# Kernel tuning notes

Measured on AMD Instinct MI355X. Metric: run time of the kernel, lower is better.

The kernel has to match this reference:

```python
import jax, jax.numpy as jnp
import numpy as np

B, S, D = 64, 2048, 64

def setup_inputs() -> dict:
    key = jax.random.key(0)
    k1, k2, k3, k4 = jax.random.split(key, 4)
    query = jax.random.normal(k1, (B, S, D), dtype=jnp.float32)
    keyt = jax.random.normal(k2, (B, S, D), dtype=jnp.float32)
    value = jax.random.normal(k3, (B, S, D), dtype=jnp.float32)
    mask = jax.random.randint(k4, (1, S, S), 0, 2, dtype=jnp.int32)
    return {"query": query, "key": keyt, "value": value, "mask": mask}

def reference(query, key, value, mask):
    # scores: [B, S, S]
    scale = jnp.sqrt(jnp.asarray(value.shape[-1], dtype=query.dtype))
    scores = jnp.einsum('bqd,bkd->bqk', query, key) / scale
    scores = jnp.where(mask == 0, jnp.asarray(-1e9, dtype=scores.dtype), scores)
    attention_weights = jax.nn.softmax(scores, axis=-1)
    # dropout p=0.0 -> identity
    context = jnp.einsum('bqk,bkd->bqd', attention_weights, value)
    return (context, attention_weights)
```

## Files before the change

### kernel.cpp

```cpp
#include <hip/hip_runtime.h>

#define NB 64
#define NS 2048
#define ND 64
#define KSTEP 64
#define NIT (NS / KSTEP)

typedef __bf16 bf16x8 __attribute__((ext_vector_type(8)));
typedef float f32x4 __attribute__((ext_vector_type(4)));
typedef unsigned int u32;
typedef u32 u32x2 __attribute__((ext_vector_type(2)));
typedef u32 u32x4 __attribute__((ext_vector_type(4)));
typedef unsigned short u16;
typedef u16 u16x8 __attribute__((ext_vector_type(8)));

#define C2F 0.18033688011112042f

__device__ __forceinline__ float fexp2(float x) {
#if __has_builtin(__builtin_amdgcn_exp2f)
  return __builtin_amdgcn_exp2f(x);
#else
  return exp2f(x);
#endif
}
__device__ __forceinline__ float flog2(float x) {
#if __has_builtin(__builtin_amdgcn_logf)
  return __builtin_amdgcn_logf(x);
#else
  return log2f(x);
#endif
}

#define TILE_BARRIER()                                   \
  do {                                                   \
    asm volatile("s_waitcnt lgkmcnt(0)" ::: "memory");   \
    __builtin_amdgcn_s_barrier();                        \
    asm volatile("" ::: "memory");                       \
  } while (0)

__device__ __forceinline__ u16 f2bs(float x) {
  __bf16 h = (__bf16)x;
  return __builtin_bit_cast(u16, h);
}

__device__ __forceinline__ bf16x8 cvt8(f32x4 a, f32x4 b) {
  bf16x8 r;
  r[0] = (__bf16)a[0]; r[1] = (__bf16)a[1]; r[2] = (__bf16)a[2]; r[3] = (__bf16)a[3];
  r[4] = (__bf16)b[0]; r[5] = (__bf16)b[1]; r[6] = (__bf16)b[2]; r[7] = (__bf16)b[3];
  return r;
}

__global__ __launch_bounds__(256) void prep_cast_k(const float* __restrict__ K,
                                                   u16* __restrict__ Kbf) {
  const size_t i = ((size_t)blockIdx.x * 256 + threadIdx.x) * 8;
  f32x4 a = __builtin_nontemporal_load((const f32x4*)(K + i));
  f32x4 b = __builtin_nontemporal_load((const f32x4*)(K + i + 4));
  *(bf16x8*)(Kbf + i) = cvt8(a, b);
}

__global__ __launch_bounds__(256) void prep_transp_v(const float* __restrict__ V,
                                                     u16* __restrict__ VT) {
  __shared__ __attribute__((aligned(16))) u16 T[64][72];
  const int b = blockIdx.x >> 5, kt = blockIdx.x & 31;
  const float* src = V + ((size_t)b * NS + kt * 64) * ND;
  {
    const int k = threadIdx.x >> 2, d0 = (threadIdx.x & 3) * 16;
    const float* p = src + (size_t)k * ND + d0;
    f32x4 a0 = __builtin_nontemporal_load((const f32x4*)p);
    f32x4 a1 = __builtin_nontemporal_load((const f32x4*)(p + 4));
    f32x4 a2 = __builtin_nontemporal_load((const f32x4*)(p + 8));
    f32x4 a3 = __builtin_nontemporal_load((const f32x4*)(p + 12));
    *(bf16x8*)&T[k][d0]     = cvt8(a0, a1);
    *(bf16x8*)&T[k][d0 + 8] = cvt8(a2, a3);
  }
  __syncthreads();
  const int d = threadIdx.x >> 2, k0 = (threadIdx.x & 3) * 16;
  u16x8 r0, r1;
#pragma unroll
  for (int j = 0; j < 8; ++j) {
    const int P0 = k0 + j, P1 = k0 + 8 + j;
    const int s0 = 32 * (P0 >> 5) + 16 * ((P0 >> 2) & 1) + 4 * ((P0 >> 3) & 3) + (P0 & 3);
    const int s1 = 32 * (P1 >> 5) + 16 * ((P1 >> 2) & 1) + 4 * ((P1 >> 3) & 3) + (P1 & 3);
    r0[j] = T[s0][d];
    r1[j] = T[s1][d];
  }
  u16* dst = VT + ((size_t)b * ND + d) * NS + kt * 64 + k0;
  *(u16x8*)dst = r0;
  *(u16x8*)(dst + 8) = r1;
}

__global__ __launch_bounds__(256) void prep_pack_mask(const int* __restrict__ M,
                                                      unsigned long long* __restrict__ Mb) {
  const size_t i = (size_t)blockIdx.x * 256 + threadIdx.x;
  const unsigned long long bal = __ballot(M[i] != 0);
  if ((threadIdx.x & 63) == 0) Mb[i >> 6] = bal;
}

template <bool PRE>
__global__ __launch_bounds__(512, 3) void DotProductAttention_22436909154804_kernel(
    const float* __restrict__ Q, const float* __restrict__ K,
    const float* __restrict__ V, const int* __restrict__ M,
    const u16* __restrict__ Kbf, const u16* __restrict__ VTbf,
    const u32* __restrict__ Mb, float* __restrict__ ctx, float* __restrict__ wts) {
  __shared__ __attribute__((aligned(16))) u16 Kt[2][64][72];
  __shared__ __attribute__((aligned(16))) u16 Vt[2][64][72];
  __shared__ float Rs[2][64];

  const int tid  = threadIdx.x;
  const int lane = tid & 63;
  const int w    = tid >> 6;
  const int wq   = w & 3;
  const int kt   = w >> 2;
  const int g    = lane >> 4;
  const int c    = lane & 15;

  const int bid = blockIdx.x;
  const int vb  = (bid & 7) * 256 + (bid >> 3);
  const int b   = vb >> 5;
  const int qt  = vb & 31;
  const int q0w = qt * 64 + wq * 16;
  const size_t bq = (size_t)b * NS;

  const float* qp = Q + (bq + q0w + c) * ND + 8 * g;
  f32x4 qa = __builtin_nontemporal_load((const f32x4*)qp);
  f32x4 qb = __builtin_nontemporal_load((const f32x4*)(qp + 4));
  const bf16x8 qf0 = cvt8(qa, qb);
  qa = __builtin_nontemporal_load((const f32x4*)(qp + 32));
  qb = __builtin_nontemporal_load((const f32x4*)(qp + 36));
  const bf16x8 qf1 = cvt8(qa, qb);

  const u16* Kbb = PRE ? (Kbf + bq * ND) : (const u16*)nullptr;
  const u16* VTb = PRE ? (VTbf + bq * ND) : (const u16*)nullptr;
  const float* Kb32 = K + bq * ND;
  const float* Vb32 = V + bq * ND;
  const int* Mr  = M + (size_t)(q0w + c) * NS + kt * 32;
  const u32* Mbr = Mb + (size_t)(q0w + c) * (NS / 32) + kt;

  const bool isK = tid < 256;
  const int st   = tid & 255;

  auto msel = [](float e, u32 mm, int idx) -> float {
    u32 keep = (u32)(((int)(mm << (31 - idx))) >> 31);
    return __uint_as_float(__float_as_uint(e) & keep);
  };

  u16x8 sp0, sp1;
  f32x4 kf0, kf1, kf2, kf3;
  auto issueK1 = [&](int kb) {
    if (PRE) {
      const int r = tid >> 3, cc = (tid & 7) * 8;
      sp0 = *(const u16x8*)(Kbb + (size_t)(kb + r) * ND + cc);
    } else if (isK) {
      const int r = st >> 2, cc = (st & 3) * 16;
      const float* p = Kb32 + (size_t)(kb + r) * ND + cc;
      kf0 = *(const f32x4*)p;       kf1 = *(const f32x4*)(p + 4);
      kf2 = *(const f32x4*)(p + 8); kf3 = *(const f32x4*)(p + 12);
    }
  };
  auto writeK1 = [&](int buf) {
    if (PRE) {
      const int r = tid >> 3, cc = (tid & 7) * 8;
      *(u16x8*)&Kt[buf][r][cc] = sp0;
    } else if (isK) {
      const int r = st >> 2, cc = (st & 3) * 16;
      *(bf16x8*)&Kt[buf][r][cc]     = cvt8(kf0, kf1);
      *(bf16x8*)&Kt[buf][r][cc + 8] = cvt8(kf2, kf3);
    }
  };
  auto issueKV = [&](int kb) {
    if (PRE) {
      if (isK) {
        const int r = st >> 2, cc = (st & 3) * 16;
        const u16* p = Kbb + (size_t)(kb + r) * ND + cc;
        sp0 = *(const u16x8*)p; sp1 = *(const u16x8*)(p + 8);
      } else {
        const int d = st >> 2, kc = (st & 3) * 16;
        const u16* p = VTb + (size_t)d * NS + kb + kc;
        sp0 = *(const u16x8*)p; sp1 = *(const u16x8*)(p + 8);
      }
    } else {
      if (isK) {
        const int r = st >> 2, cc = (st & 3) * 16;
        const float* p = Kb32 + (size_t)(kb + r) * ND + cc;
        kf0 = *(const f32x4*)p;       kf1 = *(const f32x4*)(p + 4);
        kf2 = *(const f32x4*)(p + 8); kf3 = *(const f32x4*)(p + 12);
      } else {
        const int k = st >> 2, d0 = (st & 3) * 16;
        const float* p = Vb32 + (size_t)(kb + k) * ND + d0;
        kf0 = *(const f32x4*)p;       kf1 = *(const f32x4*)(p + 4);
        kf2 = *(const f32x4*)(p + 8); kf3 = *(const f32x4*)(p + 12);
      }
    }
  };
  auto writeKV = [&](int buf) {
    if (PRE) {
      if (isK) {
        const int r = st >> 2, cc = (st & 3) * 16;
        *(u16x8*)&Kt[buf][r][cc] = sp0; *(u16x8*)&Kt[buf][r][cc + 8] = sp1;
      } else {
        const int d = st >> 2, kc = (st & 3) * 16;
        *(u16x8*)&Vt[buf][d][kc] = sp0; *(u16x8*)&Vt[buf][d][kc + 8] = sp1;
      }
    } else {
      if (isK) {
        const int r = st >> 2, cc = (st & 3) * 16;
        *(bf16x8*)&Kt[buf][r][cc]     = cvt8(kf0, kf1);
        *(bf16x8*)&Kt[buf][r][cc + 8] = cvt8(kf2, kf3);
      } else {
        const int k = st >> 2, d0 = (st & 3) * 16;
        bf16x8 v0 = cvt8(kf0, kf1), v1 = cvt8(kf2, kf3);
#pragma unroll
        for (int j = 0; j < 8; ++j) {
          Vt[buf][d0 + j][k]     = __builtin_bit_cast(u16, v0[j]);
          Vt[buf][d0 + 8 + j][k] = __builtin_bit_cast(u16, v1[j]);
        }
      }
    }
  };

  const f32x4 zz = {0.f, 0.f, 0.f, 0.f};

  float rs = 0.f;
  issueK1(0);
  writeK1(0);
  __syncthreads();
  for (int it = 0; it < NIT; ++it) {
    const int cur = it & 1, kb = it * KSTEP;
    if (it + 1 < NIT) issueK1(kb + KSTEP);
    u32 mm = 0;
    if (PRE) mm = Mbr[kb >> 5];
#pragma unroll
    for (int j = 0; j < 2; ++j) {
      bf16x8 a0 = *(const bf16x8*)&Kt[cur][kt * 32 + 16 * j + c][8 * g];
      bf16x8 a1 = *(const bf16x8*)&Kt[cur][kt * 32 + 16 * j + c][32 + 8 * g];
      f32x4 s = __builtin_amdgcn_mfma_f32_16x16x32_bf16(a0, qf0, zz, 0, 0, 0);
      s = __builtin_amdgcn_mfma_f32_16x16x32_bf16(a1, qf1, s, 0, 0, 0);
      if (PRE) {
        rs += msel(fexp2(s[0] * C2F), mm, 16 * j + 4 * g + 0)
            + msel(fexp2(s[1] * C2F), mm, 16 * j + 4 * g + 1)
            + msel(fexp2(s[2] * C2F), mm, 16 * j + 4 * g + 2)
            + msel(fexp2(s[3] * C2F), mm, 16 * j + 4 * g + 3);
      } else {
        const int4 m4 = *(const int4*)(Mr + kb + 16 * j + 4 * g);
        rs += (m4.x ? fexp2(s[0] * C2F) : 0.f)
            + (m4.y ? fexp2(s[1] * C2F) : 0.f)
            + (m4.z ? fexp2(s[2] * C2F) : 0.f)
            + (m4.w ? fexp2(s[3] * C2F) : 0.f);
      }
    }
    if (it + 1 < NIT) writeK1((it + 1) & 1);
    TILE_BARRIER();
  }
  rs += __shfl_xor(rs, 16);
  rs += __shfl_xor(rs, 32);
  issueKV(0);
  if (lane < 16) Rs[kt][wq * 16 + c] = rs;
  __syncthreads();
  const float l2inv = -flog2(Rs[0][wq * 16 + c] + Rs[1][wq * 16 + c]);
  writeKV(0);
  __syncthreads();

  f32x4 acc[4] = {zz, zz, zz, zz};
  float* wrow = wts + (bq + q0w + c) * NS + kt * 32;
  for (int it = 0; it < NIT; ++it) {
    const int cur = it & 1, kb = it * KSTEP;
    if (it + 1 < NIT) issueKV(kb + KSTEP);
    u32 mm = 0;
    if (PRE) mm = Mbr[kb >> 5];

    u32 wpk[4];
#pragma unroll
    for (int j = 0; j < 2; ++j) {
      bf16x8 a0 = *(const bf16x8*)&Kt[cur][kt * 32 + 16 * j + c][8 * g];
      bf16x8 a1 = *(const bf16x8*)&Kt[cur][kt * 32 + 16 * j + c][32 + 8 * g];
      f32x4 s = __builtin_amdgcn_mfma_f32_16x16x32_bf16(a0, qf0, zz, 0, 0, 0);
      s = __builtin_amdgcn_mfma_f32_16x16x32_bf16(a1, qf1, s, 0, 0, 0);
      float w0, w1, w2, w3;
      if (PRE) {
        w0 = msel(fexp2(fmaf(s[0], C2F, l2inv)), mm, 16 * j + 4 * g + 0);
        w1 = msel(fexp2(fmaf(s[1], C2F, l2inv)), mm, 16 * j + 4 * g + 1);
        w2 = msel(fexp2(fmaf(s[2], C2F, l2inv)), mm, 16 * j + 4 * g + 2);
        w3 = msel(fexp2(fmaf(s[3], C2F, l2inv)), mm, 16 * j + 4 * g + 3);
      } else {
        const int4 m4 = *(const int4*)(Mr + kb + 16 * j + 4 * g);
        w0 = m4.x ? fexp2(fmaf(s[0], C2F, l2inv)) : 0.f;
        w1 = m4.y ? fexp2(fmaf(s[1], C2F, l2inv)) : 0.f;
        w2 = m4.z ? fexp2(fmaf(s[2], C2F, l2inv)) : 0.f;
        w3 = m4.w ? fexp2(fmaf(s[3], C2F, l2inv)) : 0.f;
      }
      f32x4 wv = {w0, w1, w2, w3};
      __builtin_nontemporal_store(wv, (f32x4*)(wrow + kb + 16 * j + 4 * g));
      wpk[2 * j]     = (u32)f2bs(w0) | ((u32)f2bs(w1) << 16);
      wpk[2 * j + 1] = (u32)f2bs(w2) | ((u32)f2bs(w3) << 16);
    }

    u32x4 wu = {wpk[0], wpk[1], wpk[2], wpk[3]};
    bf16x8 wb = __builtin_bit_cast(bf16x8, wu);
#pragma unroll
    for (int dt = 0; dt < 4; ++dt) {
      bf16x8 va;
      if (PRE) {
        va = *(const bf16x8*)&Vt[cur][dt * 16 + c][kt * 32 + 8 * g];
      } else {
        u32x2 vlo = *(const u32x2*)&Vt[cur][dt * 16 + c][kt * 32 + 4 * g];
        u32x2 vhi = *(const u32x2*)&Vt[cur][dt * 16 + c][kt * 32 + 16 + 4 * g];
        u32x4 vau = {vlo.x, vlo.y, vhi.x, vhi.y};
        va = __builtin_bit_cast(bf16x8, vau);
      }
      acc[dt] = __builtin_amdgcn_mfma_f32_16x16x32_bf16(va, wb, acc[dt], 0, 0, 0);
    }

    if (it + 1 < NIT) writeKV((it + 1) & 1);
    TILE_BARRIER();
  }

  float* red = (float*)&Kt[0][0][0] + wq * 1088;
  if (kt == 1) {
#pragma unroll
    for (int dt = 0; dt < 4; ++dt)
      *(f32x4*)&red[c * 68 + dt * 16 + 4 * g] = acc[dt];
  }
  __syncthreads();
  if (kt == 0) {
    float* crow = ctx + (bq + q0w + c) * ND;
#pragma unroll
    for (int dt = 0; dt < 4; ++dt) {
      f32x4 vv = acc[dt] + *(const f32x4*)&red[c * 68 + dt * 16 + 4 * g];
      __builtin_nontemporal_store(vv, (f32x4*)(crow + dt * 16 + 4 * g));
    }
  }
}

extern "C" void kernel_launch(void* const* d_in, const int* in_sizes, int n_in,
                              void* d_out, int out_size, void* d_ws, size_t ws_size,
                              hipStream_t stream) {
  const float* Q = (const float*)d_in[0];
  const float* K = (const float*)d_in[1];
  const float* V = (const float*)d_in[2];
  const int*   M = (const int*)d_in[3];
  float* ctx = (float*)d_out;
  float* wts = (float*)d_out + (size_t)NB * NS * ND;

  dim3 grid(NB * (NS / 64));
  dim3 block(512);

  constexpr size_t KBF_B = (size_t)NB * NS * ND * 2;
  constexpr size_t MB_B  = (size_t)NS * NS / 8;
  u16* Kbf = (u16*)d_ws;
  u16* VTb = (u16*)((char*)d_ws + KBF_B);
  unsigned long long* Mb64 = (unsigned long long*)((char*)d_ws + 2 * KBF_B);

  if (ws_size >= 2 * KBF_B + MB_B) {
    hipLaunchKernelGGL(prep_cast_k, dim3(NB * NS * ND / 8 / 256), dim3(256), 0, stream, K, Kbf);
    hipLaunchKernelGGL(prep_transp_v, dim3(NB * (NS / 64)), dim3(256), 0, stream, V, VTb);
    hipLaunchKernelGGL(prep_pack_mask, dim3(NS * NS / 256), dim3(256), 0, stream, M, Mb64);
    hipLaunchKernelGGL(DotProductAttention_22436909154804_kernel<true>, grid, block, 0, stream,
                       Q, K, V, M, Kbf, VTb, (const u32*)Mb64, ctx, wts);
  } else {
    hipLaunchKernelGGL(DotProductAttention_22436909154804_kernel<false>, grid, block, 0, stream,
                       Q, K, V, M, (const u16*)nullptr, (const u16*)nullptr,
                       (const u32*)nullptr, ctx, wts);
  }
}
```

Baseline: 346.0 us.

## Widen pass-1 key tiles to 128 rows using both K and V smem buffers

In the precomputed-bf16 path, the row-sum pass now loads 128 key rows per iteration instead of 64. It reuses both the Kt and Vt shared buffers as a double-buffered pair, so each warp handles 64 keys per step with a two-word mask load. This halves the number of barrier-separated iterations in pass 1 and gives each thread wider 32-byte loads. The cost is more MFMA/exp work per step and more shared-memory use, with the pass-2 loaders moved below pass 1.

```diff
diff --git a/kernel.cpp b/kernel.cpp
--- a/kernel.cpp
+++ b/kernel.cpp
@@ -133,8 +133,9 @@
   const u16* VTb = PRE ? (VTbf + bq * ND) : (const u16*)nullptr;
   const float* Kb32 = K + bq * ND;
   const float* Vb32 = V + bq * ND;
-  const int* Mr  = M + (size_t)(q0w + c) * NS + kt * 32;
-  const u32* Mbr = Mb + (size_t)(q0w + c) * (NS / 32) + kt;
+  const int* Mr   = M + (size_t)(q0w + c) * NS + kt * 32;
+  const u32* MbRow = Mb + (size_t)(q0w + c) * (NS / 32);
+  const u32* Mbr   = MbRow + kt;
 
   const bool isK = tid < 256;
   const int st   = tid & 255;
@@ -144,115 +145,142 @@
     return __uint_as_float(__float_as_uint(e) & keep);
   };
 
-  u16x8 sp0, sp1;
-  f32x4 kf0, kf1, kf2, kf3;
-  auto issueK1 = [&](int kb) {
-    if (PRE) {
-      const int r = tid >> 3, cc = (tid & 7) * 8;
-      sp0 = *(const u16x8*)(Kbb + (size_t)(kb + r) * ND + cc);
-    } else if (isK) {
-      const int r = st >> 2, cc = (st & 3) * 16;
-      const float* p = Kb32 + (size_t)(kb + r) * ND + cc;
-      kf0 = *(const f32x4*)p;       kf1 = *(const f32x4*)(p + 4);
-      kf2 = *(const f32x4*)(p + 8); kf3 = *(const f32x4*)(p + 12);
-    }
-  };
-  auto writeK1 = [&](int buf) {
-    if (PRE) {
-      const int r = tid >> 3, cc = (tid & 7) * 8;
-      *(u16x8*)&Kt[buf][r][cc] = sp0;
-    } else if (isK) {
-      const int r = st >> 2, cc = (st & 3) * 16;
-      *(bf16x8*)&Kt[buf][r][cc]     = cvt8(kf0, kf1);
-      *(bf16x8*)&Kt[buf][r][cc + 8] = cvt8(kf2, kf3);
-    }
-  };
-  auto issueKV = [&](int kb) {
-    if (PRE) {
-      if (isK) {
-        const int r = st >> 2, cc = (st & 3) * 16;
-        const u16* p = Kbb + (size_t)(kb + r) * ND + cc;
-        sp0 = *(const u16x8*)p; sp1 = *(const u16x8*)(p + 8);
-      } else {
-        const int d = st >> 2, kc = (st & 3) * 16;
-        const u16* p = VTb + (size_t)d * NS + kb + kc;
-        sp0 = *(const u16x8*)p; sp1 = *(const u16x8*)(p + 8);
-      }
-    } else {
+  const f32x4 zz = {0.f, 0.f, 0.f, 0.f};
+  float rs = 0.f;
+
+  if (PRE) {
+    const int r1  = tid >> 2;
+    const int cc1 = (tid & 3) * 16;
+    u16x8 pa, pb;
+    auto issueP1 = [&](int kb) {
+      const u16* p = Kbb + (size_t)(kb + r1) * ND + cc1;
+      pa = *(const u16x8*)p;
+      pb = *(const u16x8*)(p + 8);
+    };
+    auto writeP1 = [&](int pair) {
+      u16(*dst)[72] = pair ? Vt[r1 >> 6] : Kt[r1 >> 6];
+      *(u16x8*)&dst[r1 & 63][cc1]     = pa;
+      *(u16x8*)&dst[r1 & 63][cc1 + 8] = pb;
+    };
+    issueP1(0);
+    writeP1(0);
+    __syncthreads();
+    for (int it = 0; it < 16; ++it) {
+      const int pair = it & 1;
+      if (it + 1 < 16) issueP1((it + 1) * 128);
+      const u32x2 mv = *(const u32x2*)(MbRow + it * 4 + kt * 2);
+      u16(*B)[72] = pair ? Vt[kt] : Kt[kt];
+#pragma unroll
+      for (int j = 0; j < 4; ++j) {
+        bf16x8 a0 = *(const bf16x8*)&B[16 * j + c][8 * g];
+        bf16x8 a1 = *(const bf16x8*)&B[16 * j + c][32 + 8 * g];
+        f32x4 s = __builtin_amdgcn_mfma_f32_16x16x32_bf16(a0, qf0, zz, 0, 0, 0);
+        s = __builtin_amdgcn_mfma_f32_16x16x32_bf16(a1, qf1, s, 0, 0, 0);
+        const u32 mm = (j < 2) ? mv.x : mv.y;
+        const int base = 16 * (j & 1) + 4 * g;
+        rs += msel(fexp2(s[0] * C2F), mm, base + 0)
+            + msel(fexp2(s[1] * C2F), mm, base + 1)
+            + msel(fexp2(s[2] * C2F), mm, base + 2)
+            + msel(fexp2(s[3] * C2F), mm, base + 3);
+      }
+      if (it + 1 < 16) writeP1((it + 1) & 1);
+      TILE_BARRIER();
+    }
+  } else {
+    f32x4 kf0, kf1, kf2, kf3;
+    auto issueK1 = [&](int kb) {
       if (isK) {
         const int r = st >> 2, cc = (st & 3) * 16;
         const float* p = Kb32 + (size_t)(kb + r) * ND + cc;
         kf0 = *(const f32x4*)p;       kf1 = *(const f32x4*)(p + 4);
         kf2 = *(const f32x4*)(p + 8); kf3 = *(const f32x4*)(p + 12);
-      } else {
-        const int k = st >> 2, d0 = (st & 3) * 16;
-        const float* p = Vb32 + (size_t)(kb + k) * ND + d0;
-        kf0 = *(const f32x4*)p;       kf1 = *(const f32x4*)(p + 4);
-        kf2 = *(const f32x4*)(p + 8); kf3 = *(const f32x4*)(p + 12);
-      }
-    }
-  };
-  auto writeKV = [&](int buf) {
-    if (PRE) {
-      if (isK) {
-        const int r = st >> 2, cc = (st & 3) * 16;
-        *(u16x8*)&Kt[buf][r][cc] = sp0; *(u16x8*)&Kt[buf][r][cc + 8] = sp1;
-      } else {
-        const int d = st >> 2, kc = (st & 3) * 16;
-        *(u16x8*)&Vt[buf][d][kc] = sp0; *(u16x8*)&Vt[buf][d][kc + 8] = sp1;
-      }
-    } else {
+      }
+    };
+    auto writeK1 = [&](int buf) {
       if (isK) {
         const int r = st >> 2, cc = (st & 3) * 16;
         *(bf16x8*)&Kt[buf][r][cc]     = cvt8(kf0, kf1);
         *(bf16x8*)&Kt[buf][r][cc + 8] = cvt8(kf2, kf3);
-      } else {
-        const int k = st >> 2, d0 = (st & 3) * 16;
-        bf16x8 v0 = cvt8(kf0, kf1), v1 = cvt8(kf2, kf3);
-#pragma unroll
-        for (int j = 0; j < 8; ++j) {
-          Vt[buf][d0 + j][k]     = __builtin_bit_cast(u16, v0[j]);
-          Vt[buf][d0 + 8 + j][k] = __builtin_bit_cast(u16, v1[j]);
-        }
-      }
-    }
-  };
-
-  const f32x4 zz = {0.f, 0.f, 0.f, 0.f};
-
-  float rs = 0.f;
-  issueK1(0);
-  writeK1(0);
-  __syncthreads();
-  for (int it = 0; it < NIT; ++it) {
-    const int cur = it & 1, kb = it * KSTEP;
-    if (it + 1 < NIT) issueK1(kb + KSTEP);
-    u32 mm = 0;
-    if (PRE) mm = Mbr[kb >> 5];
-#pragma unroll
-    for (int j = 0; j < 2; ++j) {
-      bf16x8 a0 = *(const bf16x8*)&Kt[cur][kt * 32 + 16 * j + c][8 * g];
-      bf16x8 a1 = *(const bf16x8*)&Kt[cur][kt * 32 + 16 * j + c][32 + 8 * g];
-      f32x4 s = __builtin_amdgcn_mfma_f32_16x16x32_bf16(a0, qf0, zz, 0, 0, 0);
-      s = __builtin_amdgcn_mfma_f32_16x16x32_bf16(a1, qf1, s, 0, 0, 0);
-      if (PRE) {
-        rs += msel(fexp2(s[0] * C2F), mm, 16 * j + 4 * g + 0)
-            + msel(fexp2(s[1] * C2F), mm, 16 * j + 4 * g + 1)
-            + msel(fexp2(s[2] * C2F), mm, 16 * j + 4 * g + 2)
-            + msel(fexp2(s[3] * C2F), mm, 16 * j + 4 * g + 3);
-      } else {
+      }
+    };
+    issueK1(0);
+    writeK1(0);
+    __syncthreads();
+    for (int it = 0; it < NIT; ++it) {
+      const int cur = it & 1, kb = it * KSTEP;
+      if (it + 1 < NIT) issueK1(kb + KSTEP);
+#pragma unroll
+      for (int j = 0; j < 2; ++j) {
+        bf16x8 a0 = *(const bf16x8*)&Kt[cur][kt * 32 + 16 * j + c][8 * g];
+        bf16x8 a1 = *(const bf16x8*)&Kt[cur][kt * 32 + 16 * j + c][32 + 8 * g];
+        f32x4 s = __builtin_amdgcn_mfma_f32_16x16x32_bf16(a0, qf0, zz, 0, 0, 0);
+        s = __builtin_amdgcn_mfma_f32_16x16x32_bf16(a1, qf1, s, 0, 0, 0);
         const int4 m4 = *(const int4*)(Mr + kb + 16 * j + 4 * g);
         rs += (m4.x ? fexp2(s[0] * C2F) : 0.f)
             + (m4.y ? fexp2(s[1] * C2F) : 0.f)
             + (m4.z ? fexp2(s[2] * C2F) : 0.f)
             + (m4.w ? fexp2(s[3] * C2F) : 0.f);
       }
-    }
-    if (it + 1 < NIT) writeK1((it + 1) & 1);
-    TILE_BARRIER();
+      if (it + 1 < NIT) writeK1((it + 1) & 1);
+      TILE_BARRIER();
+    }
   }
   rs += __shfl_xor(rs, 16);
   rs += __shfl_xor(rs, 32);
+
+  u16x8 sp0, sp1;
+  f32x4 kf0, kf1, kf2, kf3;
+  auto issueKV = [&](int kb) {
+    if (PRE) {
+      if (isK) {
+        const int r = st >> 2, cc = (st & 3) * 16;
+        const u16* p = Kbb + (size_t)(kb + r) * ND + cc;
+        sp0 = *(const u16x8*)p; sp1 = *(const u16x8*)(p + 8);
+      } else {
+        const int d = st >> 2, kc = (st & 3) * 16;
+        const u16* p = VTb + (size_t)d * NS + kb + kc;
+        sp0 = *(const u16x8*)p; sp1 = *(const u16x8*)(p + 8);
+      }
+    } else {
+      if (isK) {
+        const int r = st >> 2, cc = (st & 3) * 16;
+        const float* p = Kb32 + (size_t)(kb + r) * ND + cc;
+        kf0 = *(const f32x4*)p;       kf1 = *(const f32x4*)(p + 4);
+        kf2 = *(const f32x4*)(p + 8); kf3 = *(const f32x4*)(p + 12);
+      } else {
+        const int k = st >> 2, d0 = (st & 3) * 16;
+        const float* p = Vb32 + (size_t)(kb + k) * ND + d0;
+        kf0 = *(const f32x4*)p;       kf1 = *(const f32x4*)(p + 4);
+        kf2 = *(const f32x4*)(p + 8); kf3 = *(const f32x4*)(p + 12);
+      }
+    }
+  };
+  auto writeKV = [&](int buf) {
+    if (PRE) {
+      if (isK) {
+        const int r = st >> 2, cc = (st & 3) * 16;
+        *(u16x8*)&Kt[buf][r][cc] = sp0; *(u16x8*)&Kt[buf][r][cc + 8] = sp1;
+      } else {
+        const int d = st >> 2, kc = (st & 3) * 16;
+        *(u16x8*)&Vt[buf][d][kc] = sp0; *(u16x8*)&Vt[buf][d][kc + 8] = sp1;
+      }
+    } else {
+      if (isK) {
+        const int r = st >> 2, cc = (st & 3) * 16;
+        *(bf16x8*)&Kt[buf][r][cc]     = cvt8(kf0, kf1);
+        *(bf16x8*)&Kt[buf][r][cc + 8] = cvt8(kf2, kf3);
+      } else {
+        const int k = st >> 2, d0 = (st & 3) * 16;
+        bf16x8 v0 = cvt8(kf0, kf1), v1 = cvt8(kf2, kf3);
+#pragma unroll
+        for (int j = 0; j < 8; ++j) {
+          Vt[buf][d0 + j][k]     = __builtin_bit_cast(u16, v0[j]);
+          Vt[buf][d0 + 8 + j][k] = __builtin_bit_cast(u16, v1[j]);
+        }
+      }
+    }
+  };
+
   issueKV(0);
   if (lane < 16) Rs[kt][wq * 16 + c] = rs;
   __syncthreads();
```

After: 336.1 us (median of 2 runs). -2.8%, faster.

## Read bf16 K directly from global in row-sum pass, splitting keys per kt

Applied to the files above, without the earlier changes.

In the precomputed-bf16 path, the first (row-sum) pass no longer stages K tiles through double-buffered LDS with barriers. Each kt half now loads its own contiguous 1024-key range straight from global memory into MFMA operands and reads the packed mask words sequentially. The aim is to drop the LDS writes, reads and per-iteration barriers from this pass. The cost is uncoalesced, L2-dependent global loads with nothing overlapping their latency. The exp2/log2 helpers are also switched from amdgcn builtins to the standard exp2f/log2f, which may add range-handling instructions.

```diff
diff --git a/kernel.cpp b/kernel.cpp
--- a/kernel.cpp
+++ b/kernel.cpp
@@ -16,20 +16,8 @@
 
 #define C2F 0.18033688011112042f
 
-__device__ __forceinline__ float fexp2(float x) {
-#if __has_builtin(__builtin_amdgcn_exp2f)
-  return __builtin_amdgcn_exp2f(x);
-#else
-  return exp2f(x);
-#endif
-}
-__device__ __forceinline__ float flog2(float x) {
-#if __has_builtin(__builtin_amdgcn_logf)
-  return __builtin_amdgcn_logf(x);
-#else
-  return log2f(x);
-#endif
-}
+__device__ __forceinline__ float fexp2(float x) { return exp2f(x); }
+__device__ __forceinline__ float flog2(float x) { return log2f(x); }
 
 #define TILE_BARRIER()                                   \
   do {                                                   \
@@ -133,8 +121,9 @@
   const u16* VTb = PRE ? (VTbf + bq * ND) : (const u16*)nullptr;
   const float* Kb32 = K + bq * ND;
   const float* Vb32 = V + bq * ND;
-  const int* Mr  = M + (size_t)(q0w + c) * NS + kt * 32;
-  const u32* Mbr = Mb + (size_t)(q0w + c) * (NS / 32) + kt;
+  const int* Mr    = M + (size_t)(q0w + c) * NS + kt * 32;
+  const u32* MbRow = Mb + (size_t)(q0w + c) * (NS / 32);
+  const u32* Mbr   = MbRow + kt;
 
   const bool isK = tid < 256;
   const int st   = tid & 255;
@@ -144,115 +133,123 @@
     return __uint_as_float(__float_as_uint(e) & keep);
   };
 
-  u16x8 sp0, sp1;
-  f32x4 kf0, kf1, kf2, kf3;
-  auto issueK1 = [&](int kb) {
-    if (PRE) {
-      const int r = tid >> 3, cc = (tid & 7) * 8;
-      sp0 = *(const u16x8*)(Kbb + (size_t)(kb + r) * ND + cc);
-    } else if (isK) {
-      const int r = st >> 2, cc = (st & 3) * 16;
-      const float* p = Kb32 + (size_t)(kb + r) * ND + cc;
-      kf0 = *(const f32x4*)p;       kf1 = *(const f32x4*)(p + 4);
-      kf2 = *(const f32x4*)(p + 8); kf3 = *(const f32x4*)(p + 12);
-    }
-  };
-  auto writeK1 = [&](int buf) {
-    if (PRE) {
-      const int r = tid >> 3, cc = (tid & 7) * 8;
-      *(u16x8*)&Kt[buf][r][cc] = sp0;
-    } else if (isK) {
-      const int r = st >> 2, cc = (st & 3) * 16;
-      *(bf16x8*)&Kt[buf][r][cc]     = cvt8(kf0, kf1);
-      *(bf16x8*)&Kt[buf][r][cc + 8] = cvt8(kf2, kf3);
-    }
-  };
-  auto issueKV = [&](int kb) {
-    if (PRE) {
-      if (isK) {
-        const int r = st >> 2, cc = (st & 3) * 16;
-        const u16* p = Kbb + (size_t)(kb + r) * ND + cc;
-        sp0 = *(const u16x8*)p; sp1 = *(const u16x8*)(p + 8);
-      } else {
-        const int d = st >> 2, kc = (st & 3) * 16;
-        const u16* p = VTb + (size_t)d * NS + kb + kc;
-        sp0 = *(const u16x8*)p; sp1 = *(const u16x8*)(p + 8);
-      }
-    } else {
-      if (isK) {
-        const int r = st >> 2, cc = (st & 3) * 16;
-        const float* p = Kb32 + (size_t)(kb + r) * ND + cc;
-        kf0 = *(const f32x4*)p;       kf1 = *(const f32x4*)(p + 4);
-        kf2 = *(const f32x4*)(p + 8); kf3 = *(const f32x4*)(p + 12);
-      } else {
-        const int k = st >> 2, d0 = (st & 3) * 16;
-        const float* p = Vb32 + (size_t)(kb + k) * ND + d0;
-        kf0 = *(const f32x4*)p;       kf1 = *(const f32x4*)(p + 4);
-        kf2 = *(const f32x4*)(p + 8); kf3 = *(const f32x4*)(p + 12);
-      }
-    }
-  };
-  auto writeKV = [&](int buf) {
-    if (PRE) {
-      if (isK) {
-        const int r = st >> 2, cc = (st & 3) * 16;
-        *(u16x8*)&Kt[buf][r][cc] = sp0; *(u16x8*)&Kt[buf][r][cc + 8] = sp1;
-      } else {
-        const int d = st >> 2, kc = (st & 3) * 16;
-        *(u16x8*)&Vt[buf][d][kc] = sp0; *(u16x8*)&Vt[buf][d][kc + 8] = sp1;
-      }
-    } else {
-      if (isK) {
-        const int r = st >> 2, cc = (st & 3) * 16;
-        *(bf16x8*)&Kt[buf][r][cc]     = cvt8(kf0, kf1);
-        *(bf16x8*)&Kt[buf][r][cc + 8] = cvt8(kf2, kf3);
-      } else {
-        const int k = st >> 2, d0 = (st & 3) * 16;
-        bf16x8 v0 = cvt8(kf0, kf1), v1 = cvt8(kf2, kf3);
-#pragma unroll
-        for (int j = 0; j < 8; ++j) {
-          Vt[buf][d0 + j][k]     = __builtin_bit_cast(u16, v0[j]);
-          Vt[buf][d0 + 8 + j][k] = __builtin_bit_cast(u16, v1[j]);
-        }
-      }
-    }
-  };
-
   const f32x4 zz = {0.f, 0.f, 0.f, 0.f};
-
   float rs = 0.f;
-  issueK1(0);
-  writeK1(0);
-  __syncthreads();
-  for (int it = 0; it < NIT; ++it) {
-    const int cur = it & 1, kb = it * KSTEP;
-    if (it + 1 < NIT) issueK1(kb + KSTEP);
-    u32 mm = 0;
-    if (PRE) mm = Mbr[kb >> 5];
-#pragma unroll
-    for (int j = 0; j < 2; ++j) {
-      bf16x8 a0 = *(const bf16x8*)&Kt[cur][kt * 32 + 16 * j + c][8 * g];
-      bf16x8 a1 = *(const bf16x8*)&Kt[cur][kt * 32 + 16 * j + c][32 + 8 * g];
-      f32x4 s = __builtin_amdgcn_mfma_f32_16x16x32_bf16(a0, qf0, zz, 0, 0, 0);
-      s = __builtin_amdgcn_mfma_f32_16x16x32_bf16(a1, qf1, s, 0, 0, 0);
-      if (PRE) {
+
+  if (PRE) {
+    const u16* Kh = Kbb + (size_t)kt * 1024 * ND;
+    const u32* Mh = MbRow + kt * 32;
+    for (int it = 0; it < 32; ++it) {
+      const int k0 = it * 32;
+      const u32 mm = Mh[it];
+#pragma unroll
+      for (int j = 0; j < 2; ++j) {
+        const u16* kr = Kh + (size_t)(k0 + 16 * j + c) * ND + 8 * g;
+        bf16x8 a0 = *(const bf16x8*)kr;
+        bf16x8 a1 = *(const bf16x8*)(kr + 32);
+        f32x4 s = __builtin_amdgcn_mfma_f32_16x16x32_bf16(a0, qf0, zz, 0, 0, 0);
+        s = __builtin_amdgcn_mfma_f32_16x16x32_bf16(a1, qf1, s, 0, 0, 0);
         rs += msel(fexp2(s[0] * C2F), mm, 16 * j + 4 * g + 0)
             + msel(fexp2(s[1] * C2F), mm, 16 * j + 4 * g + 1)
             + msel(fexp2(s[2] * C2F), mm, 16 * j + 4 * g + 2)
             + msel(fexp2(s[3] * C2F), mm, 16 * j + 4 * g + 3);
-      } else {
+      }
+    }
+  } else {
+    f32x4 kf0, kf1, kf2, kf3;
+    auto issueK1 = [&](int kb) {
+      if (isK) {
+        const int r = st >> 2, cc = (st & 3) * 16;
+        const float* p = Kb32 + (size_t)(kb + r) * ND + cc;
+        kf0 = *(const f32x4*)p;       kf1 = *(const f32x4*)(p + 4);
+        kf2 = *(const f32x4*)(p + 8); kf3 = *(const f32x4*)(p + 12);
+      }
+    };
+    auto writeK1 = [&](int buf) {
+      if (isK) {
+        const int r = st >> 2, cc = (st & 3) * 16;
+        *(bf16x8*)&Kt[buf][r][cc]     = cvt8(kf0, kf1);
+        *(bf16x8*)&Kt[buf][r][cc + 8] = cvt8(kf2, kf3);
+      }
+    };
+    issueK1(0);
+    writeK1(0);
+    __syncthreads();
+    for (int it = 0; it < NIT; ++it) {
+      const int cur = it & 1, kb = it * KSTEP;
+      if (it + 1 < NIT) issueK1(kb + KSTEP);
+#pragma unroll
+      for (int j = 0; j < 2; ++j) {
+        bf16x8 a0 = *(const bf16x8*)&Kt[cur][kt * 32 + 16 * j + c][8 * g];
+        bf16x8 a1 = *(const bf16x8*)&Kt[cur][kt * 32 + 16 * j + c][32 + 8 * g];
+        f32x4 s = __builtin_amdgcn_mfma_f32_16x16x32_bf16(a0, qf0, zz, 0, 0, 0);
+        s = __builtin_amdgcn_mfma_f32_16x16x32_bf16(a1, qf1, s, 0, 0, 0);
         const int4 m4 = *(const int4*)(Mr + kb + 16 * j + 4 * g);
         rs += (m4.x ? fexp2(s[0] * C2F) : 0.f)
             + (m4.y ? fexp2(s[1] * C2F) : 0.f)
             + (m4.z ? fexp2(s[2] * C2F) : 0.f)
             + (m4.w ? fexp2(s[3] * C2F) : 0.f);
       }
-    }
-    if (it + 1 < NIT) writeK1((it + 1) & 1);
-    TILE_BARRIER();
+      if (it + 1 < NIT) writeK1((it + 1) & 1);
+      TILE_BARRIER();
+    }
   }
   rs += __shfl_xor(rs, 16);
   rs += __shfl_xor(rs, 32);
+
+  u16x8 sp0, sp1;
+  f32x4 kf0, kf1, kf2, kf3;
+  auto issueKV = [&](int kb) {
+    if (PRE) {
+      if (isK) {
+        const int r = st >> 2, cc = (st & 3) * 16;
+        const u16* p = Kbb + (size_t)(kb + r) * ND + cc;
+        sp0 = *(const u16x8*)p; sp1 = *(const u16x8*)(p + 8);
+      } else {
+        const int d = st >> 2, kc = (st & 3) * 16;
+        const u16* p = VTb + (size_t)d * NS + kb + kc;
+        sp0 = *(const u16x8*)p; sp1 = *(const u16x8*)(p + 8);
+      }
+    } else {
+      if (isK) {
+        const int r = st >> 2, cc = (st & 3) * 16;
+        const float* p = Kb32 + (size_t)(kb + r) * ND + cc;
+        kf0 = *(const f32x4*)p;       kf1 = *(const f32x4*)(p + 4);
+        kf2 = *(const f32x4*)(p + 8); kf3 = *(const f32x4*)(p + 12);
+      } else {
+        const int k = st >> 2, d0 = (st & 3) * 16;
+        const float* p = Vb32 + (size_t)(kb + k) * ND + d0;
+        kf0 = *(const f32x4*)p;       kf1 = *(const f32x4*)(p + 4);
+        kf2 = *(const f32x4*)(p + 8); kf3 = *(const f32x4*)(p + 12);
+      }
+    }
+  };
+  auto writeKV = [&](int buf) {
+    if (PRE) {
+      if (isK) {
+        const int r = st >> 2, cc = (st & 3) * 16;
+        *(u16x8*)&Kt[buf][r][cc] = sp0; *(u16x8*)&Kt[buf][r][cc + 8] = sp1;
+      } else {
+        const int d = st >> 2, kc = (st & 3) * 16;
+        *(u16x8*)&Vt[buf][d][kc] = sp0; *(u16x8*)&Vt[buf][d][kc + 8] = sp1;
+      }
+    } else {
+      if (isK) {
+        const int r = st >> 2, cc = (st & 3) * 16;
+        *(bf16x8*)&Kt[buf][r][cc]     = cvt8(kf0, kf1);
+        *(bf16x8*)&Kt[buf][r][cc + 8] = cvt8(kf2, kf3);
+      } else {
+        const int k = st >> 2, d0 = (st & 3) * 16;
+        bf16x8 v0 = cvt8(kf0, kf1), v1 = cvt8(kf2, kf3);
+#pragma unroll
+        for (int j = 0; j < 8; ++j) {
+          Vt[buf][d0 + j][k]     = __builtin_bit_cast(u16, v0[j]);
+          Vt[buf][d0 + 8 + j][k] = __builtin_bit_cast(u16, v1[j]);
+        }
+      }
+    }
+  };
+
   issueKV(0);
   if (lane < 16) Rs[kt][wq * 16 + c] = rs;
   __syncthreads();
```

Measured after the change: 528.2 us. 52.7% more time.
